# Kernel optimization log

Hardware: AMD Instinct MI355X
Metric: run time of the kernel (lower is better)

The kernel has to match this reference:

```python
import jax, jax.numpy as jnp
import numpy as np

VOCAB = 100000
EMBED = 128
N_INNER = VOCAB - 1
MAX_PATH = 20
BATCH = 32768


def setup_inputs() -> dict:
    key = jax.random.key(0)
    k1, k2, k3, k4, k5, k6, k7 = jax.random.split(key, 7)
    center = jax.random.randint(k1, (BATCH,), 0, VOCAB)
    target = jax.random.randint(k2, (BATCH,), 0, VOCAB)
    # embedding table (module inits uniform(-0.5/d, 0.5/d)); inner vectors init zero,
    # but we use small random values so gradients/scores are non-trivial.
    init_range = 0.5 / EMBED
    in_emb = jax.random.uniform(k3, (VOCAB, EMBED), jnp.float32, -init_range, init_range)
    inner_vec = jax.random.normal(k4, (N_INNER, EMBED), jnp.float32) * 0.01
    # Huffman buffers: per-word path lengths between 8 and MAX_PATH, padded with 0.
    lengths = jax.random.randint(k5, (VOCAB, 1), 8, MAX_PATH + 1)          # (V,1)
    pos = jnp.arange(MAX_PATH)[None, :]                                     # (1,L)
    masks = (pos < lengths).astype(jnp.float32)                             # (V,L)
    paths = jax.random.randint(k6, (VOCAB, MAX_PATH), 0, N_INNER) * (pos < lengths)
    # codes are +/-1 on valid positions (word2vec sign labels), 0 on padding
    codes = (2.0 * jax.random.randint(k7, (VOCAB, MAX_PATH), 0, 2).astype(jnp.float32) - 1.0) * masks
    return {"center": center, "target": target, "in_emb": in_emb,
            "inner_vec": inner_vec, "paths": paths, "codes": codes, "masks": masks}


def reference(center, target, in_emb, inner_vec, paths, codes, masks):
    h = in_emb[center]                      # (B, D) center word vectors
    p = paths[target]                       # (B, L) inner-node ids along Huffman path
    c = codes[target]                       # (B, L) +/-1 direction labels
    m = masks[target]                       # (B, L) valid-position mask
    iv = inner_vec[p]                       # (B, L, D) gathered inner-node vectors
    scores = jnp.einsum('bld,bd->bl', iv, h)            # batched matvec
    log_probs = jax.nn.log_sigmoid(c * scores)          # (B, L)
    loss = -(log_probs * m).sum(axis=1)                 # masked path sum
    return loss.mean()
```

## Files before the change

### kernel.cpp

```cpp
#include <hip/hip_runtime.h>

#define VOCAB 100000
#define EMBED 128
#define MAX_PATH 20
#define BATCH 32768
#define WPB 4
#define NBLOCKS (BATCH / WPB)

__global__ __launch_bounds__(256, 8) void hs_loss_kernel(
    const int* __restrict__ center, const int* __restrict__ target,
    const float* __restrict__ in_emb, const float* __restrict__ inner_vec,
    const int* __restrict__ paths, const float* __restrict__ codes,
    float* __restrict__ partials)
{
    __shared__ float4 lds_buf[WPB * 256];
    __shared__ float  ws[WPB];

    const int wave = threadIdx.x >> 6;
    const int lane = threadIdx.x & 63;
    const int g    = lane >> 4;
    const int gl   = lane & 15;
    const int b = blockIdx.x * WPB + wave;

    const int c = center[b];
    const int t = target[b];

    const float4* hp = (const float4*)(in_emb + (size_t)c * EMBED);
    const float4 h0 = hp[gl];
    const float4 h1 = hp[gl + 16];

    const int base = t * MAX_PATH + g;
    int   p[5];
    float cd[5];
    #pragma unroll
    for (int j = 0; j < 5; ++j) {
        p[j]  = paths[base + 4 * j];
        cd[j] = codes[base + 4 * j];
    }
    const bool do3 = __ballot(cd[3] != 0.f) != 0ull;
    const bool do4 = __ballot(cd[4] != 0.f) != 0ull;

    const float4* v0 = (const float4*)(inner_vec + (size_t)p[0] * EMBED);
    const float4 r00 = v0[gl], r01 = v0[gl + 16];
    const float4* v1 = (const float4*)(inner_vec + (size_t)p[1] * EMBED);
    const float4 r10 = v1[gl], r11 = v1[gl + 16];
    const float4* v2 = (const float4*)(inner_vec + (size_t)p[2] * EMBED);
    const float4 r20 = v2[gl], r21 = v2[gl + 16];

    float4* myl = lds_buf + wave * 256;
    if (do3) {
        const float* src = inner_vec + (size_t)p[3] * EMBED + 4 * gl;
        __builtin_amdgcn_global_load_lds(
            (const __attribute__((address_space(1))) unsigned int*)(src),
            (__attribute__((address_space(3))) unsigned int*)(myl),
            16, 0, 0);
        __builtin_amdgcn_global_load_lds(
            (const __attribute__((address_space(1))) unsigned int*)(src + 64),
            (__attribute__((address_space(3))) unsigned int*)(myl + 64),
            16, 0, 0);
    }
    if (do4) {
        const float* src = inner_vec + (size_t)p[4] * EMBED + 4 * gl;
        __builtin_amdgcn_global_load_lds(
            (const __attribute__((address_space(1))) unsigned int*)(src),
            (__attribute__((address_space(3))) unsigned int*)(myl + 128),
            16, 0, 0);
        __builtin_amdgcn_global_load_lds(
            (const __attribute__((address_space(1))) unsigned int*)(src + 64),
            (__attribute__((address_space(3))) unsigned int*)(myl + 192),
            16, 0, 0);
    }

    float acc = 0.f;
    #pragma unroll
    for (int j = 0; j < 3; ++j) {
        const float4 a0 = (j == 0) ? r00 : (j == 1) ? r10 : r20;
        const float4 a1 = (j == 0) ? r01 : (j == 1) ? r11 : r21;
        float d = h0.x * a0.x;
        d = fmaf(h0.y, a0.y, d);
        d = fmaf(h0.z, a0.z, d);
        d = fmaf(h0.w, a0.w, d);
        float e = h1.x * a1.x;
        e = fmaf(h1.y, a1.y, e);
        e = fmaf(h1.z, a1.z, e);
        e = fmaf(h1.w, a1.w, e);
        d += e;
        d += __shfl_xor(d, 1, 64);
        d += __shfl_xor(d, 2, 64);
        d += __shfl_xor(d, 4, 64);
        d += __shfl_xor(d, 8, 64);
        const float x  = cd[j] * d;
        const float ls = fminf(x, 0.f) - __logf(1.f + __expf(-fabsf(x)));
        acc = fmaf(fabsf(cd[j]), ls, acc);
    }

    __builtin_amdgcn_s_waitcnt(0xF70);
    __builtin_amdgcn_sched_barrier(0);

    #pragma unroll
    for (int j = 3; j < 5; ++j) {
        if (j == 3 && !do3) continue;
        if (j == 4 && !do4) continue;
        const float4 a0 = myl[(j - 3) * 128 + lane];
        const float4 a1 = myl[(j - 3) * 128 + 64 + lane];
        float d = h0.x * a0.x;
        d = fmaf(h0.y, a0.y, d);
        d = fmaf(h0.z, a0.z, d);
        d = fmaf(h0.w, a0.w, d);
        float e = h1.x * a1.x;
        e = fmaf(h1.y, a1.y, e);
        e = fmaf(h1.z, a1.z, e);
        e = fmaf(h1.w, a1.w, e);
        d += e;
        d += __shfl_xor(d, 1, 64);
        d += __shfl_xor(d, 2, 64);
        d += __shfl_xor(d, 4, 64);
        d += __shfl_xor(d, 8, 64);
        const float x  = cd[j] * d;
        const float ls = fminf(x, 0.f) - __logf(1.f + __expf(-fabsf(x)));
        acc = fmaf(fabsf(cd[j]), ls, acc);
    }

    acc += __shfl_xor(acc, 16, 64);
    acc += __shfl_xor(acc, 32, 64);

    if (lane == 0) ws[wave] = -acc;
    __syncthreads();
    if (threadIdx.x == 0) {
        partials[blockIdx.x] = ws[0] + ws[1] + ws[2] + ws[3];
    }
}

__global__ __launch_bounds__(256) void hs_reduce_kernel(
    const float* __restrict__ partials, float* __restrict__ out)
{
    const float4* p4 = (const float4*)partials;
    float s = 0.f;
    #pragma unroll
    for (int i = 0; i < NBLOCKS / 4 / 256; ++i) {
        const float4 v = p4[i * 256 + threadIdx.x];
        s += (v.x + v.y) + (v.z + v.w);
    }
    #pragma unroll
    for (int off = 32; off; off >>= 1) s += __shfl_xor(s, off, 64);
    __shared__ float ws[4];
    const int wave = threadIdx.x >> 6;
    const int lane = threadIdx.x & 63;
    if (lane == 0) ws[wave] = s;
    __syncthreads();
    if (threadIdx.x == 0) {
        out[0] = (ws[0] + ws[1] + ws[2] + ws[3]) / (float)BATCH;
    }
}

extern "C" void kernel_launch(void* const* d_in, const int* in_sizes, int n_in,
                              void* d_out, int out_size, void* d_ws, size_t ws_size,
                              hipStream_t stream) {
    const int*   center    = (const int*)d_in[0];
    const int*   target    = (const int*)d_in[1];
    const float* in_emb    = (const float*)d_in[2];
    const float* inner_vec = (const float*)d_in[3];
    const int*   paths     = (const int*)d_in[4];
    const float* codes     = (const float*)d_in[5];
    float* out = (float*)d_out;
    float* partials = (float*)d_ws;

    hs_loss_kernel<<<NBLOCKS, 256, 0, stream>>>(
        center, target, in_emb, inner_vec, paths, codes, partials);
    hs_reduce_kernel<<<1, 256, 0, stream>>>(partials, out);
}
```

Baseline: 157.2 us.

## Software-pipeline multiple batch elements per wave with async LDS prefetch

Each wave now processes 16 batch elements instead of one, with path and code metadata prefetched two elements ahead and gathered vectors prefetched one ahead into double-buffered LDS via global_load_lds, using counted vmcnt waits. The center embedding is also loaded through LDS. This aims to hide gather latency within a wave instead of relying on occupancy. The trade-off is heavy register use for the per-element arrays and fewer blocks. It also always processes 5 path positions per lane without the skip for empty tails.

```diff
diff --git a/kernel.cpp b/kernel.cpp
--- a/kernel.cpp
+++ b/kernel.cpp
@@ -4,121 +4,118 @@
 #define EMBED 128
 #define MAX_PATH 20
 #define BATCH 32768
-#define WPB 4
-#define NBLOCKS (BATCH / WPB)
+#define WPB 2
+#define EPW 16
+#define NBLK (BATCH / (WPB * EPW))
 
-__global__ __launch_bounds__(256, 8) void hs_loss_kernel(
+constexpr unsigned VMW(unsigned n) {
+    return 0x0F70u | (n & 0xFu) | ((n >> 4) << 14);
+}
+
+#define GLDS(SRC, DST)                                                        \
+    __builtin_amdgcn_global_load_lds(                                         \
+        (const __attribute__((address_space(1))) unsigned int*)(SRC),         \
+        (__attribute__((address_space(3))) unsigned int*)(DST), 16, 0, 0)
+
+__global__ __launch_bounds__(128, 4) void hs_loss_kernel(
     const int* __restrict__ center, const int* __restrict__ target,
     const float* __restrict__ in_emb, const float* __restrict__ inner_vec,
     const int* __restrict__ paths, const float* __restrict__ codes,
     float* __restrict__ partials)
 {
-    __shared__ float4 lds_buf[WPB * 256];
+    __shared__ float4 lds4[WPB][2][448];
     __shared__ float  ws[WPB];
 
     const int wave = threadIdx.x >> 6;
     const int lane = threadIdx.x & 63;
     const int g    = lane >> 4;
     const int gl   = lane & 15;
-    const int b = blockIdx.x * WPB + wave;
+    const int w    = blockIdx.x * WPB + wave;
+    const int b0   = w * EPW;
 
-    const int c = center[b];
-    const int t = target[b];
+    const int cvec = center[b0 + (lane & 15)];
+    const int tvec = target[b0 + (lane & 15)];
 
-    const float4* hp = (const float4*)(in_emb + (size_t)c * EMBED);
-    const float4 h0 = hp[gl];
-    const float4 h1 = hp[gl + 16];
+    int   p[EPW][5];
+    float cd[EPW][5];
+    float4 rg[EPW][4];
 
-    const int base = t * MAX_PATH + g;
-    int   p[5];
-    float cd[5];
-    #pragma unroll
-    for (int j = 0; j < 5; ++j) {
-        p[j]  = paths[base + 4 * j];
-        cd[j] = codes[base + 4 * j];
-    }
-    const bool do3 = __ballot(cd[3] != 0.f) != 0ull;
-    const bool do4 = __ballot(cd[4] != 0.f) != 0ull;
+    auto issue_meta = [&](int e) {
+        const int t_e = __shfl(tvec, e, 64);
+        const int mb  = t_e * MAX_PATH + g;
+        #pragma unroll
+        for (int j = 0; j < 5; ++j) {
+            p[e][j]  = paths[mb + 4 * j];
+            cd[e][j] = codes[mb + 4 * j];
+        }
+    };
 
-    const float4* v0 = (const float4*)(inner_vec + (size_t)p[0] * EMBED);
-    const float4 r00 = v0[gl], r01 = v0[gl + 16];
-    const float4* v1 = (const float4*)(inner_vec + (size_t)p[1] * EMBED);
-    const float4 r10 = v1[gl], r11 = v1[gl + 16];
-    const float4* v2 = (const float4*)(inner_vec + (size_t)p[2] * EMBED);
-    const float4 r20 = v2[gl], r21 = v2[gl + 16];
-
-    float4* myl = lds_buf + wave * 256;
-    if (do3) {
-        const float* src = inner_vec + (size_t)p[3] * EMBED + 4 * gl;
-        __builtin_amdgcn_global_load_lds(
-            (const __attribute__((address_space(1))) unsigned int*)(src),
-            (__attribute__((address_space(3))) unsigned int*)(myl),
-            16, 0, 0);
-        __builtin_amdgcn_global_load_lds(
-            (const __attribute__((address_space(1))) unsigned int*)(src + 64),
-            (__attribute__((address_space(3))) unsigned int*)(myl + 64),
-            16, 0, 0);
-    }
-    if (do4) {
-        const float* src = inner_vec + (size_t)p[4] * EMBED + 4 * gl;
-        __builtin_amdgcn_global_load_lds(
-            (const __attribute__((address_space(1))) unsigned int*)(src),
-            (__attribute__((address_space(3))) unsigned int*)(myl + 128),
-            16, 0, 0);
-        __builtin_amdgcn_global_load_lds(
-            (const __attribute__((address_space(1))) unsigned int*)(src + 64),
-            (__attribute__((address_space(3))) unsigned int*)(myl + 192),
-            16, 0, 0);
-    }
+    auto issue_G = [&](int e) {
+        const int c_e = __shfl(cvec, e, 64);
+        const float4* v0 = (const float4*)(inner_vec + (size_t)p[e][0] * EMBED);
+        const float4* v1 = (const float4*)(inner_vec + (size_t)p[e][1] * EMBED);
+        rg[e][0] = v0[gl];  rg[e][1] = v0[gl + 16];
+        rg[e][2] = v1[gl];  rg[e][3] = v1[gl + 16];
+        float4* dst = &lds4[wave][e & 1][0];
+        const float* hsrc = in_emb + (size_t)c_e * EMBED + 4 * (lane & 31);
+        GLDS(hsrc, dst);
+        #pragma unroll
+        for (int cn = 0; cn < 3; ++cn) {
+            const float* src = inner_vec + (size_t)p[e][cn + 2] * EMBED + 4 * gl;
+            GLDS(src,      dst + 64 + cn * 128);
+            GLDS(src + 64, dst + 64 + cn * 128 + 64);
+        }
+    };
 
     float acc = 0.f;
-    #pragma unroll
-    for (int j = 0; j < 3; ++j) {
-        const float4 a0 = (j == 0) ? r00 : (j == 1) ? r10 : r20;
-        const float4 a1 = (j == 0) ? r01 : (j == 1) ? r11 : r21;
-        float d = h0.x * a0.x;
-        d = fmaf(h0.y, a0.y, d);
-        d = fmaf(h0.z, a0.z, d);
-        d = fmaf(h0.w, a0.w, d);
-        float e = h1.x * a1.x;
-        e = fmaf(h1.y, a1.y, e);
-        e = fmaf(h1.z, a1.z, e);
-        e = fmaf(h1.w, a1.w, e);
-        d += e;
-        d += __shfl_xor(d, 1, 64);
-        d += __shfl_xor(d, 2, 64);
-        d += __shfl_xor(d, 4, 64);
-        d += __shfl_xor(d, 8, 64);
-        const float x  = cd[j] * d;
-        const float ls = fminf(x, 0.f) - __logf(1.f + __expf(-fabsf(x)));
-        acc = fmaf(fabsf(cd[j]), ls, acc);
-    }
+    auto do_compute = [&](int k) {
+        const float4* buf = &lds4[wave][k & 1][0];
+        const float4 h0 = buf[gl];
+        const float4 h1 = buf[gl + 16];
+        #pragma unroll
+        for (int j = 0; j < 5; ++j) {
+            float4 a0, a1;
+            if (j < 2) { a0 = rg[k][2 * j]; a1 = rg[k][2 * j + 1]; }
+            else {
+                a0 = buf[64 + (j - 2) * 128 + lane];
+                a1 = buf[64 + (j - 2) * 128 + 64 + lane];
+            }
+            float d = h0.x * a0.x;
+            d = fmaf(h0.y, a0.y, d);
+            d = fmaf(h0.z, a0.z, d);
+            d = fmaf(h0.w, a0.w, d);
+            float e2 = h1.x * a1.x;
+            e2 = fmaf(h1.y, a1.y, e2);
+            e2 = fmaf(h1.z, a1.z, e2);
+            e2 = fmaf(h1.w, a1.w, e2);
+            d += e2;
+            d += __shfl_xor(d, 1, 64);
+            d += __shfl_xor(d, 2, 64);
+            d += __shfl_xor(d, 4, 64);
+            d += __shfl_xor(d, 8, 64);
+            const float x  = cd[k][j] * d;
+            const float ls = fminf(x, 0.f) - __logf(1.f + __expf(-fabsf(x)));
+            acc = fmaf(fabsf(cd[k][j]), ls, acc);
+        }
+    };
 
-    __builtin_amdgcn_s_waitcnt(0xF70);
+    issue_meta(0);
+    issue_meta(1);
+    __builtin_amdgcn_sched_barrier(0);
+    issue_G(0);
     __builtin_amdgcn_sched_barrier(0);
 
     #pragma unroll
-    for (int j = 3; j < 5; ++j) {
-        if (j == 3 && !do3) continue;
-        if (j == 4 && !do4) continue;
-        const float4 a0 = myl[(j - 3) * 128 + lane];
-        const float4 a1 = myl[(j - 3) * 128 + 64 + lane];
-        float d = h0.x * a0.x;
-        d = fmaf(h0.y, a0.y, d);
-        d = fmaf(h0.z, a0.z, d);
-        d = fmaf(h0.w, a0.w, d);
-        float e = h1.x * a1.x;
-        e = fmaf(h1.y, a1.y, e);
-        e = fmaf(h1.z, a1.z, e);
-        e = fmaf(h1.w, a1.w, e);
-        d += e;
-        d += __shfl_xor(d, 1, 64);
-        d += __shfl_xor(d, 2, 64);
-        d += __shfl_xor(d, 4, 64);
-        d += __shfl_xor(d, 8, 64);
-        const float x  = cd[j] * d;
-        const float ls = fminf(x, 0.f) - __logf(1.f + __expf(-fabsf(x)));
-        acc = fmaf(fabsf(cd[j]), ls, acc);
+    for (int k = 0; k < EPW; ++k) {
+        if (k + 2 < EPW) issue_meta(k + 2);
+        __builtin_amdgcn_sched_barrier(0);
+        if (k + 1 < EPW) issue_G(k + 1);
+        __builtin_amdgcn_sched_barrier(0);
+        if      (k < EPW - 2) __builtin_amdgcn_s_waitcnt(VMW(21));
+        else if (k < EPW - 1) __builtin_amdgcn_s_waitcnt(VMW(11));
+        else                  __builtin_amdgcn_s_waitcnt(VMW(0));
+        __builtin_amdgcn_sched_barrier(0);
+        do_compute(k);
     }
 
     acc += __shfl_xor(acc, 16, 64);
@@ -127,7 +124,7 @@
     if (lane == 0) ws[wave] = -acc;
     __syncthreads();
     if (threadIdx.x == 0) {
-        partials[blockIdx.x] = ws[0] + ws[1] + ws[2] + ws[3];
+        partials[blockIdx.x] = ws[0] + ws[1];
     }
 }
 
@@ -135,12 +132,8 @@
     const float* __restrict__ partials, float* __restrict__ out)
 {
     const float4* p4 = (const float4*)partials;
-    float s = 0.f;
-    #pragma unroll
-    for (int i = 0; i < NBLOCKS / 4 / 256; ++i) {
-        const float4 v = p4[i * 256 + threadIdx.x];
-        s += (v.x + v.y) + (v.z + v.w);
-    }
+    const float4 v = p4[threadIdx.x];
+    float s = (v.x + v.y) + (v.z + v.w);
     #pragma unroll
     for (int off = 32; off; off >>= 1) s += __shfl_xor(s, off, 64);
     __shared__ float ws[4];
@@ -165,7 +158,7 @@
     float* out = (float*)d_out;
     float* partials = (float*)d_ws;
 
-    hs_loss_kernel<<<NBLOCKS, 256, 0, stream>>>(
+    hs_loss_kernel<<<NBLK, 128, 0, stream>>>(
         center, target, in_emb, inner_vec, paths, codes, partials);
     hs_reduce_kernel<<<1, 256, 0, stream>>>(partials, out);
 }
```

Measured after the change: 161.5 us. 2.7% more time.
